# Performance work log

Hardware: AMD Instinct MI355X
Metric: run time of the kernel (lower is better)

## Reference

```python
import jax, jax.numpy as jnp
import numpy as np

NUM_BINS = 256


def setup_inputs() -> dict:
    key = jax.random.key(0)
    x = jax.random.uniform(key, (16, 3, 1024, 1024), dtype=jnp.float32)
    return {"x": x}


def reference(x) -> jnp.ndarray:
    B, C, H, W = x.shape
    # Quantize to NUM_BINS levels (values in [0,1] so truncation == torch .long())
    x_flat = jnp.clip(x, 0.0, 1.0).reshape(B, C, H * W)
    x_q = jnp.clip((x_flat * (NUM_BINS - 1)).astype(jnp.int32), 0, NUM_BINS - 1)
    # Per-(B,C) histogram via a single flat scatter-add: offset each (b,c)
    # slice into its own NUM_BINS-wide segment of one 1-D buffer.
    offsets = (jnp.arange(B * C, dtype=jnp.int32) * NUM_BINS).reshape(B, C, 1)
    flat_idx = (x_q + offsets).reshape(-1)
    hist = jnp.zeros(B * C * NUM_BINS, dtype=jnp.float32).at[flat_idx].add(1.0)
    hist = hist.reshape(B, C, NUM_BINS)
    # CDF, normalized by total count (clamped at 1 to avoid div-by-zero)
    cdf = jnp.cumsum(hist, axis=2)
    cdf = cdf / jnp.maximum(cdf[:, :, -1:], 1.0)
    # Remap each pixel through its channel's CDF
    y_flat = jnp.take_along_axis(cdf, x_q, axis=2)
    return y_flat.reshape(B, C, H, W).astype(x.dtype)
```

## Files before the change

### kernel.cpp

```cpp
#include <hip/hip_runtime.h>

#define NB 256
#define NCH 48
#define HW (1024*1024)
#define BLOCKS_PER_CH 64
#define THREADS 256
#define NWAVE (THREADS / 64)

__device__ __forceinline__ int quant255(float v) {
    v = fminf(fmaxf(v, 0.0f), 1.0f);
    int q = (int)(v * 255.0f);
    q = q < 0 ? 0 : q;
    q = q > 255 ? 255 : q;
    return q;
}

__global__ __launch_bounds__(THREADS) void hist_quant_kernel(
    const float* __restrict__ x, unsigned int* __restrict__ ghist,
    unsigned int* __restrict__ q) {
    __shared__ unsigned int lh[NWAVE][NB];
    const int t = threadIdx.x;
    const int w = t >> 6;
    for (int i = t; i < NWAVE * NB; i += THREADS)
        ((unsigned int*)lh)[i] = 0u;
    __syncthreads();

    const int ch  = blockIdx.x / BLOCKS_PER_CH;
    const int blk = blockIdx.x % BLOCKS_PER_CH;

    const float4* xp = (const float4*)(x + (size_t)ch * HW);
    unsigned int* qp = q + (size_t)ch * (HW / 4);
    const int n4 = (HW / 4) / BLOCKS_PER_CH;
    const int base = blk * n4;

    for (int i = base + t; i < base + n4; i += THREADS) {
        float4 v = xp[i];
        int q0 = quant255(v.x), q1 = quant255(v.y);
        int q2 = quant255(v.z), q3 = quant255(v.w);
        atomicAdd(&lh[w][q0], 1u);
        atomicAdd(&lh[w][q1], 1u);
        atomicAdd(&lh[w][q2], 1u);
        atomicAdd(&lh[w][q3], 1u);
        qp[i] = (unsigned)q0 | ((unsigned)q1 << 8)
              | ((unsigned)q2 << 16) | ((unsigned)q3 << 24);
    }
    __syncthreads();
    unsigned int s = lh[0][t] + lh[1][t] + lh[2][t] + lh[3][t];
    if (s != 0u)
        atomicAdd(&ghist[ch * NB + t], s);
}

__global__ __launch_bounds__(THREADS) void cdf_remap_kernel(
    const unsigned int* __restrict__ q, const unsigned int* __restrict__ ghist,
    float* __restrict__ y) {
    __shared__ float sbuf[NB];
    __shared__ float lc[NB];
    const int t = threadIdx.x;
    const int ch  = blockIdx.x / BLOCKS_PER_CH;
    const int blk = blockIdx.x % BLOCKS_PER_CH;

    sbuf[t] = (float)ghist[ch * NB + t];
    __syncthreads();
    for (int off = 1; off < NB; off <<= 1) {
        float add = (t >= off) ? sbuf[t - off] : 0.0f;
        __syncthreads();
        sbuf[t] += add;
        __syncthreads();
    }
    float total = sbuf[NB - 1];
    lc[t] = sbuf[t] / fmaxf(total, 1.0f);
    __syncthreads();

    const uint4* qp = (const uint4*)(q + (size_t)ch * (HW / 4));
    float4*      yp = (float4*)(y + (size_t)ch * HW);
    const int n16 = (HW / 16) / BLOCKS_PER_CH;
    const int base = blk * n16;

    for (int i = base + t; i < base + n16; i += THREADS) {
        uint4 pv = qp[i];
        const unsigned pk[4] = { pv.x, pv.y, pv.z, pv.w };
        #pragma unroll
        for (int j = 0; j < 4; ++j) {
            unsigned p = pk[j];
            float4 o = make_float4(lc[p & 255], lc[(p >> 8) & 255],
                                   lc[(p >> 16) & 255], lc[p >> 24]);
            yp[i * 4 + j] = o;
        }
    }
}

extern "C" void kernel_launch(void* const* d_in, const int* in_sizes, int n_in,
                              void* d_out, int out_size, void* d_ws, size_t ws_size,
                              hipStream_t stream) {
    const float* x = (const float*)d_in[0];
    float* y = (float*)d_out;

    unsigned int* ghist = (unsigned int*)d_ws;
    unsigned int* q     = (unsigned int*)((char*)d_ws + 256 * 1024);

    hipMemsetAsync(ghist, 0, NCH * NB * sizeof(unsigned int), stream);

    hist_quant_kernel<<<NCH * BLOCKS_PER_CH, THREADS, 0, stream>>>(x, ghist, q);
    cdf_remap_kernel <<<NCH * BLOCKS_PER_CH, THREADS, 0, stream>>>(q, ghist, y);
}
```

Baseline: 396.8 us.

## Fuse histogram and remap into one persistent kernel with grid barrier

Replaces the two-pass design with a single kernel. Each block keeps its quantized packed pixels in LDS and registers, adds its partial histogram, then waits at a global atomic grid barrier before building the CDF and writing outputs. This removes the write and reread of the intermediate quantized buffer and one kernel launch. The cost is that all 1536 blocks must be co-resident (occupancy of at least 6 per CU on a 256-CU assumption) and spin on a barrier; if the occupancy check fails, the old two-kernel path runs instead. The fallback remap loop is also changed from uint4 loads to scalar word loads.

```diff
diff --git a/kernel.cpp b/kernel.cpp
--- a/kernel.cpp
+++ b/kernel.cpp
@@ -3,9 +3,14 @@
 #define NB 256
 #define NCH 48
 #define HW (1024*1024)
-#define BLOCKS_PER_CH 64
+#define WPC (HW / 4)
+#define BPC 32
+#define GRID (NCH * BPC)
 #define THREADS 256
-#define NWAVE (THREADS / 64)
+#define KTOT 32
+#define KLDS 6
+#define KREG (KTOT - KLDS)
+#define FB_BPC 64
 
 __device__ __forceinline__ int quant255(float v) {
     v = fminf(fmaxf(v, 0.0f), 1.0f);
@@ -15,49 +20,119 @@
     return q;
 }
 
+__device__ __forceinline__ unsigned quant_pack(float4 v, unsigned* lh, int w) {
+    int q0 = quant255(v.x), q1 = quant255(v.y);
+    int q2 = quant255(v.z), q3 = quant255(v.w);
+    atomicAdd(&lh[w * NB + q0], 1u);
+    atomicAdd(&lh[w * NB + q1], 1u);
+    atomicAdd(&lh[w * NB + q2], 1u);
+    atomicAdd(&lh[w * NB + q3], 1u);
+    return (unsigned)q0 | ((unsigned)q1 << 8)
+         | ((unsigned)q2 << 16) | ((unsigned)q3 << 24);
+}
+
+__global__ __launch_bounds__(THREADS, 6) void fused_he_kernel(
+    const float* __restrict__ x, unsigned int* __restrict__ ghist,
+    unsigned int* __restrict__ bar, float* __restrict__ y) {
+    __shared__ unsigned int sq[KLDS * THREADS];
+    __shared__ unsigned int lh[4 * NB];
+
+    const int t  = threadIdx.x;
+    const int w  = t >> 6;
+    const int ch  = blockIdx.x / BPC;
+    const int blk = blockIdx.x % BPC;
+
+    for (int i = t; i < 4 * NB; i += THREADS) lh[i] = 0u;
+    __syncthreads();
+
+    const float4* xp = (const float4*)x + (size_t)ch * WPC
+                       + (size_t)blk * (KTOT * THREADS);
+
+    for (int k = 0; k < KLDS; ++k) {
+        float4 v = xp[k * THREADS + t];
+        sq[k * THREADS + t] = quant_pack(v, lh, w);
+    }
+    unsigned int qpk[KREG];
+    #pragma unroll
+    for (int k = 0; k < KREG; ++k) {
+        float4 v = xp[(KLDS + k) * THREADS + t];
+        qpk[k] = quant_pack(v, lh, w);
+    }
+    __syncthreads();
+
+    unsigned int s = lh[t] + lh[NB + t] + lh[2 * NB + t] + lh[3 * NB + t];
+    atomicAdd(&ghist[ch * NB + t], s);
+    __threadfence();
+    __syncthreads();
+
+    if (t == 0) {
+        atomicAdd(bar, 1u);
+        while (atomicAdd(bar, 0u) < (unsigned)GRID)
+            __builtin_amdgcn_s_sleep(8);
+    }
+    __syncthreads();
+
+    float* sbuf = (float*)lh;
+    float* lut  = (float*)lh + NB;
+    sbuf[t] = (float)atomicAdd(&ghist[ch * NB + t], 0u);
+    __syncthreads();
+    for (int off = 1; off < NB; off <<= 1) {
+        float add = (t >= off) ? sbuf[t - off] : 0.0f;
+        __syncthreads();
+        sbuf[t] += add;
+        __syncthreads();
+    }
+    float total = sbuf[NB - 1];
+    lut[t] = sbuf[t] / fmaxf(total, 1.0f);
+    __syncthreads();
+
+    float4* yp = (float4*)y + (size_t)ch * WPC + (size_t)blk * (KTOT * THREADS);
+    for (int k = 0; k < KLDS; ++k) {
+        unsigned p = sq[k * THREADS + t];
+        yp[k * THREADS + t] = make_float4(lut[p & 255], lut[(p >> 8) & 255],
+                                          lut[(p >> 16) & 255], lut[p >> 24]);
+    }
+    #pragma unroll
+    for (int k = 0; k < KREG; ++k) {
+        unsigned p = qpk[k];
+        yp[(KLDS + k) * THREADS + t] = make_float4(lut[p & 255], lut[(p >> 8) & 255],
+                                                   lut[(p >> 16) & 255], lut[p >> 24]);
+    }
+}
+
 __global__ __launch_bounds__(THREADS) void hist_quant_kernel(
     const float* __restrict__ x, unsigned int* __restrict__ ghist,
     unsigned int* __restrict__ q) {
-    __shared__ unsigned int lh[NWAVE][NB];
+    __shared__ unsigned int lh[4 * NB];
     const int t = threadIdx.x;
     const int w = t >> 6;
-    for (int i = t; i < NWAVE * NB; i += THREADS)
-        ((unsigned int*)lh)[i] = 0u;
+    for (int i = t; i < 4 * NB; i += THREADS) lh[i] = 0u;
     __syncthreads();
 
-    const int ch  = blockIdx.x / BLOCKS_PER_CH;
-    const int blk = blockIdx.x % BLOCKS_PER_CH;
-
+    const int ch  = blockIdx.x / FB_BPC;
+    const int blk = blockIdx.x % FB_BPC;
     const float4* xp = (const float4*)(x + (size_t)ch * HW);
-    unsigned int* qp = q + (size_t)ch * (HW / 4);
-    const int n4 = (HW / 4) / BLOCKS_PER_CH;
+    unsigned int* qp = q + (size_t)ch * WPC;
+    const int n4 = WPC / FB_BPC;
     const int base = blk * n4;
 
     for (int i = base + t; i < base + n4; i += THREADS) {
         float4 v = xp[i];
-        int q0 = quant255(v.x), q1 = quant255(v.y);
-        int q2 = quant255(v.z), q3 = quant255(v.w);
-        atomicAdd(&lh[w][q0], 1u);
-        atomicAdd(&lh[w][q1], 1u);
-        atomicAdd(&lh[w][q2], 1u);
-        atomicAdd(&lh[w][q3], 1u);
-        qp[i] = (unsigned)q0 | ((unsigned)q1 << 8)
-              | ((unsigned)q2 << 16) | ((unsigned)q3 << 24);
+        qp[i] = quant_pack(v, lh, w);
     }
     __syncthreads();
-    unsigned int s = lh[0][t] + lh[1][t] + lh[2][t] + lh[3][t];
-    if (s != 0u)
-        atomicAdd(&ghist[ch * NB + t], s);
+    unsigned int s = lh[t] + lh[NB + t] + lh[2 * NB + t] + lh[3 * NB + t];
+    if (s) atomicAdd(&ghist[ch * NB + t], s);
 }
 
 __global__ __launch_bounds__(THREADS) void cdf_remap_kernel(
     const unsigned int* __restrict__ q, const unsigned int* __restrict__ ghist,
     float* __restrict__ y) {
     __shared__ float sbuf[NB];
-    __shared__ float lc[NB];
+    __shared__ float lut[NB];
     const int t = threadIdx.x;
-    const int ch  = blockIdx.x / BLOCKS_PER_CH;
-    const int blk = blockIdx.x % BLOCKS_PER_CH;
+    const int ch  = blockIdx.x / FB_BPC;
+    const int blk = blockIdx.x % FB_BPC;
 
     sbuf[t] = (float)ghist[ch * NB + t];
     __syncthreads();
@@ -68,24 +143,17 @@
         __syncthreads();
     }
     float total = sbuf[NB - 1];
-    lc[t] = sbuf[t] / fmaxf(total, 1.0f);
+    lut[t] = sbuf[t] / fmaxf(total, 1.0f);
     __syncthreads();
 
-    const uint4* qp = (const uint4*)(q + (size_t)ch * (HW / 4));
-    float4*      yp = (float4*)(y + (size_t)ch * HW);
-    const int n16 = (HW / 16) / BLOCKS_PER_CH;
-    const int base = blk * n16;
-
-    for (int i = base + t; i < base + n16; i += THREADS) {
-        uint4 pv = qp[i];
-        const unsigned pk[4] = { pv.x, pv.y, pv.z, pv.w };
-        #pragma unroll
-        for (int j = 0; j < 4; ++j) {
-            unsigned p = pk[j];
-            float4 o = make_float4(lc[p & 255], lc[(p >> 8) & 255],
-                                   lc[(p >> 16) & 255], lc[p >> 24]);
-            yp[i * 4 + j] = o;
-        }
+    const unsigned int* qp = q + (size_t)ch * WPC;
+    float4*             yp = (float4*)(y + (size_t)ch * HW);
+    const int n4 = WPC / FB_BPC;
+    const int base = blk * n4;
+    for (int i = base + t; i < base + n4; i += THREADS) {
+        unsigned p = qp[i];
+        yp[i] = make_float4(lut[p & 255], lut[(p >> 8) & 255],
+                            lut[(p >> 16) & 255], lut[p >> 24]);
     }
 }
 
@@ -96,10 +164,20 @@
     float* y = (float*)d_out;
 
     unsigned int* ghist = (unsigned int*)d_ws;
+    unsigned int* bar   = (unsigned int*)((char*)d_ws + 60 * 1024);
     unsigned int* q     = (unsigned int*)((char*)d_ws + 256 * 1024);
 
-    hipMemsetAsync(ghist, 0, NCH * NB * sizeof(unsigned int), stream);
+    hipMemsetAsync(d_ws, 0, 64 * 1024, stream);
 
-    hist_quant_kernel<<<NCH * BLOCKS_PER_CH, THREADS, 0, stream>>>(x, ghist, q);
-    cdf_remap_kernel <<<NCH * BLOCKS_PER_CH, THREADS, 0, stream>>>(q, ghist, y);
+    int occ = 0;
+    hipError_t qe = hipOccupancyMaxActiveBlocksPerMultiprocessor(
+        &occ, fused_he_kernel, THREADS, 0);
+    bool fused_ok = (qe == hipSuccess) && (occ >= GRID / 256);
+
+    if (fused_ok) {
+        fused_he_kernel<<<GRID, THREADS, 0, stream>>>(x, ghist, bar, y);
+    } else {
+        hist_quant_kernel<<<NCH * FB_BPC, THREADS, 0, stream>>>(x, ghist, q);
+        cdf_remap_kernel <<<NCH * FB_BPC, THREADS, 0, stream>>>(q, ghist, y);
+    }
 }
```

New measurement: 368.3 us. 7.2% less time.
